# Kernel tuning notes

Hardware: AMD Instinct MI355X
Metric: run time of the kernel (lower is better)

The kernel has to match this reference:

```python
import jax, jax.numpy as jnp
import numpy as np

H = 16      # num_attention_heads
HKV = 4     # num_key_value_heads
HIDDEN = 1024
HEAD_DIM = HIDDEN // H  # 64
ROPE_BASE = 10000.0


def _rope(x):
    # Rotate-half RoPE applied over the FULL projected last dim, matching the
    # module which applies self._rope before splitting into heads.
    B, S, D = x.shape
    half = D // 2
    inv_freq = 1.0 / (ROPE_BASE ** (jnp.arange(half, dtype=jnp.float32) / half))
    ang = jnp.arange(S, dtype=jnp.float32)[:, None] * inv_freq[None, :]  # [S, half]
    cos, sin = jnp.cos(ang), jnp.sin(ang)
    x1, x2 = x[..., :half], x[..., half:]
    return jnp.concatenate([x1 * cos - x2 * sin, x2 * cos + x1 * sin], axis=-1)


def _rmsnorm(x):
    # F.rms_norm with no weight: x / sqrt(mean(x^2) + eps)
    eps = jnp.finfo(x.dtype).eps
    return x * jax.lax.rsqrt(jnp.mean(x * x, axis=-1, keepdims=True) + eps)


def setup_inputs() -> dict:
    key = jax.random.key(0)
    ks = jax.random.split(key, 10)
    B, S = 2, 2048
    kv_dim = HKV * HEAD_DIM
    sc = 0.02
    return {
        "hidden_state": jax.random.normal(ks[0], (B, S, HIDDEN), dtype=jnp.float32),
        "attention_mask": jnp.zeros((B, S, S), dtype=jnp.float32),
        "Wq": jax.random.normal(ks[1], (HIDDEN, HIDDEN), dtype=jnp.float32) * sc,
        "bq": jnp.zeros((HIDDEN,), dtype=jnp.float32),
        "Wk": jax.random.normal(ks[2], (HIDDEN, kv_dim), dtype=jnp.float32) * sc,
        "bk": jnp.zeros((kv_dim,), dtype=jnp.float32),
        "Wv": jax.random.normal(ks[3], (HIDDEN, kv_dim), dtype=jnp.float32) * sc,
        "bv": jnp.zeros((kv_dim,), dtype=jnp.float32),
        "Wo": jax.random.normal(ks[4], (HIDDEN, HIDDEN), dtype=jnp.float32) * sc,
        "bo": jnp.zeros((HIDDEN,), dtype=jnp.float32),
    }


def reference(hidden_state, attention_mask, Wq, bq, Wk, bk, Wv, bv, Wo, bo):
    B, S, _ = hidden_state.shape
    G = H // HKV  # query heads per kv head
    d = HEAD_DIM

    q = hidden_state @ Wq + bq            # [B,S,H*d]
    k = hidden_state @ Wk + bk            # [B,S,Hkv*d]
    v = hidden_state @ Wv + bv            # [B,S,Hkv*d]

    q = _rope(q)
    k = _rope(k)

    # split heads; repeat_interleave of KV over groups == grouping Q heads as [Hkv, G]
    q = q.reshape(B, S, H, d).transpose(0, 2, 1, 3).reshape(B, HKV, G, S, d)
    k = k.reshape(B, S, HKV, d).transpose(0, 2, 1, 3)   # [B,Hkv,S,d]
    v = v.reshape(B, S, HKV, d).transpose(0, 2, 1, 3)   # [B,Hkv,S,d]

    q = _rmsnorm(q)
    k = _rmsnorm(k)

    scale = d ** 0.5
    scores = jnp.einsum('bkgqd,bksd->bkgqs', q, k) / scale  # [B,Hkv,G,S,S]
    scores = scores + attention_mask[:, None, None, :, :]
    attn = jax.nn.softmax(scores, axis=-1)
    out = jnp.einsum('bkgqs,bksd->bkgqd', attn, v)          # [B,Hkv,G,S,d]

    out = out.reshape(B, H, S, d).transpose(0, 2, 1, 3).reshape(B, S, H * d)
    return out @ Wo + bo
```

## Files before the change

### kernel.cpp

```cpp
#include <hip/hip_runtime.h>
#include <cmath>

#define SEQ 2048
#define BATCH 2
#define HID 1024
#define NH 16
#define NKV 4
#define DH 64
#define KVDIM 256
#define K32C 32

typedef __attribute__((ext_vector_type(8))) short bf16x8;
typedef __attribute__((ext_vector_type(4))) float f32x4;

static __device__ __forceinline__ unsigned short f2bf(float x) {
  union { float f; unsigned u; } v; v.f = x;
  unsigned r = v.u + 0x7fffu + ((v.u >> 16) & 1u);
  return (unsigned short)(r >> 16);
}
static __device__ __forceinline__ float bf2f(unsigned short h) {
  union { unsigned u; float f; } v; v.u = ((unsigned)h) << 16;
  return v.f;
}
static __device__ __forceinline__ void gl_lds16(const unsigned short* g, unsigned short* l) {
  __builtin_amdgcn_global_load_lds(
      (const __attribute__((address_space(1))) unsigned int*)g,
      (__attribute__((address_space(3))) unsigned int*)l, 16, 0, 0);
}

template<bool HILO>
__global__ __launch_bounds__(256) void pack_a_kernel(
    const float* __restrict__ A, unsigned short* __restrict__ hi,
    unsigned short* __restrict__ lo) {
  int gid = blockIdx.x * 256 + threadIdx.x;
  int lane = gid & 63;
  int k32 = (gid >> 6) & 31;
  int m16 = gid >> 11;
  int quad = lane >> 4, l16 = lane & 15;
  const float* src = A + (size_t)(m16 * 16 + l16) * 1024 + k32 * 32 + quad * 8;
  float4 a0 = *(const float4*)src;
  float4 a1 = *(const float4*)(src + 4);
  float v[8] = {a0.x, a0.y, a0.z, a0.w, a1.x, a1.y, a1.z, a1.w};
  unsigned short h[8], l[8];
#pragma unroll
  for (int j = 0; j < 8; ++j) {
    h[j] = f2bf(v[j]);
    if (HILO) l[j] = f2bf(v[j] - bf2f(h[j]));
  }
  *(bf16x8*)(hi + (size_t)gid * 8) = *(bf16x8*)h;
  if (HILO) *(bf16x8*)(lo + (size_t)gid * 8) = *(bf16x8*)l;
}

__global__ __launch_bounds__(256) void pack_a_norm_kernel(
    const float* __restrict__ A, const float* __restrict__ lpart,
    unsigned short* __restrict__ hi, unsigned short* __restrict__ lo) {
  int gid = blockIdx.x * 256 + threadIdx.x;
  int lane = gid & 63;
  int k32 = (gid >> 6) & 31;
  int m16 = gid >> 11;
  int quad = lane >> 4, l16 = lane & 15;
  int m = m16 * 16 + l16;
  int b = m >> 11, s = m & 2047;
  int k0 = k32 * 32 + quad * 8;
  int h = k0 >> 6;
  float inv = 1.0f / lpart[(size_t)(b * NH + h) * SEQ + s];
  const float* src = A + (size_t)m * 1024 + k0;
  float4 a0 = *(const float4*)src;
  float4 a1 = *(const float4*)(src + 4);
  float v[8] = {a0.x, a0.y, a0.z, a0.w, a1.x, a1.y, a1.z, a1.w};
  unsigned short hh[8], ll[8];
#pragma unroll
  for (int j = 0; j < 8; ++j) {
    float x = v[j] * inv;
    hh[j] = f2bf(x);
    ll[j] = f2bf(x - bf2f(hh[j]));
  }
  *(bf16x8*)(hi + (size_t)gid * 8) = *(bf16x8*)hh;
  *(bf16x8*)(lo + (size_t)gid * 8) = *(bf16x8*)ll;
}

template<bool HILO>
__global__ __launch_bounds__(256) void pack_b_kernel(
    const float* __restrict__ W, unsigned short* __restrict__ hi,
    unsigned short* __restrict__ lo, int Nsrc) {
  int gid = blockIdx.x * 256 + threadIdx.x;
  int lane = gid & 63;
  int k32 = (gid >> 6) & 31;
  int n16 = gid >> 11;
  int quad = lane >> 4, l16 = lane & 15;
  int n = n16 * 16 + l16, k = k32 * 32 + quad * 8;
  unsigned short h[8], l[8];
#pragma unroll
  for (int j = 0; j < 8; ++j) {
    float v = W[(size_t)(k + j) * Nsrc + n];
    h[j] = f2bf(v);
    if (HILO) l[j] = f2bf(v - bf2f(h[j]));
  }
  *(bf16x8*)(hi + (size_t)gid * 8) = *(bf16x8*)h;
  if (HILO) *(bf16x8*)(lo + (size_t)gid * 8) = *(bf16x8*)l;
}

__global__ __launch_bounds__(256) void bias_cat_kernel(
    const float* __restrict__ bq, const float* __restrict__ bk,
    const float* __restrict__ bv, float* __restrict__ dst) {
  int n = blockIdx.x * 256 + threadIdx.x;
  if (n < 1536)
    dst[n] = (n < 1024) ? bq[n] : (n < 1280 ? bk[n - 1024] : bv[n - 1280]);
}

template<int CHAINS, bool OUTBF16>
__global__ __launch_bounds__(256) void gemm_pk_kernel(
    const unsigned short* __restrict__ Ah, const unsigned short* __restrict__ Al,
    const unsigned short* __restrict__ Bh, const unsigned short* __restrict__ Bl,
    const float* __restrict__ bias, void* __restrict__ Cout, int N) {
  constexpr int NCH = (CHAINS == 3) ? 2 : 1;
  __shared__ unsigned short Asm[NCH][4 * 512];
  __shared__ unsigned short Bsm[NCH][8 * 512];
  const int tid = threadIdx.x;
  const int wave = tid >> 6, lane = tid & 63;
  const int wr = wave >> 1, wc = wave & 1;
  const int quad = lane >> 4, l16 = lane & 15;
  const size_t abase = ((size_t)(blockIdx.y * 4 + wave) * K32C) * 64 + lane;
  const size_t bbase0 = ((size_t)(blockIdx.x * 8 + wave) * K32C) * 64 + lane;
  const size_t bbase1 = ((size_t)(blockIdx.x * 8 + wave + 4) * K32C) * 64 + lane;
  f32x4 acc[2][4] = {};
  for (int k32 = 0; k32 < K32C; ++k32) {
    __syncthreads();
    gl_lds16(Ah + (abase + (size_t)k32 * 64) * 8, &Asm[0][wave * 512]);
    gl_lds16(Bh + (bbase0 + (size_t)k32 * 64) * 8, &Bsm[0][wave * 512]);
    gl_lds16(Bh + (bbase1 + (size_t)k32 * 64) * 8, &Bsm[0][(wave + 4) * 512]);
    if (CHAINS == 3) {
      gl_lds16(Al + (abase + (size_t)k32 * 64) * 8, &Asm[1][wave * 512]);
      gl_lds16(Bl + (bbase0 + (size_t)k32 * 64) * 8, &Bsm[1][wave * 512]);
      gl_lds16(Bl + (bbase1 + (size_t)k32 * 64) * 8, &Bsm[1][(wave + 4) * 512]);
    }
    __syncthreads();
    bf16x8 af[2][NCH], bfr[4][NCH];
#pragma unroll
    for (int mt = 0; mt < 2; ++mt)
#pragma unroll
      for (int ch = 0; ch < NCH; ++ch)
        af[mt][ch] = *(const bf16x8*)&Asm[ch][((wr * 2 + mt) * 64 + lane) * 8];
#pragma unroll
    for (int nt = 0; nt < 4; ++nt)
#pragma unroll
      for (int ch = 0; ch < NCH; ++ch)
        bfr[nt][ch] = *(const bf16x8*)&Bsm[ch][((wc * 4 + nt) * 64 + lane) * 8];
#pragma unroll
    for (int mt = 0; mt < 2; ++mt)
#pragma unroll
      for (int nt = 0; nt < 4; ++nt) {
        acc[mt][nt] = __builtin_amdgcn_mfma_f32_16x16x32_bf16(af[mt][0], bfr[nt][0], acc[mt][nt], 0, 0, 0);
        if (CHAINS == 3) {
          acc[mt][nt] = __builtin_amdgcn_mfma_f32_16x16x32_bf16(af[mt][1], bfr[nt][0], acc[mt][nt], 0, 0, 0);
          acc[mt][nt] = __builtin_amdgcn_mfma_f32_16x16x32_bf16(af[mt][0], bfr[nt][1], acc[mt][nt], 0, 0, 0);
        }
      }
  }
  const int n0 = blockIdx.x * 128 + wc * 64;
  const int m0 = blockIdx.y * 64 + wr * 32;
#pragma unroll
  for (int mt = 0; mt < 2; ++mt)
#pragma unroll
    for (int nt = 0; nt < 4; ++nt)
#pragma unroll
      for (int r = 0; r < 4; ++r) {
        int gm = m0 + mt * 16 + quad * 4 + r;
        int n = n0 + nt * 16 + l16;
        float v = acc[mt][nt][r] + bias[n];
        if (OUTBF16)
          ((unsigned short*)Cout)[(size_t)gm * N + n] = f2bf(v);
        else
          ((float*)Cout)[(size_t)gm * N + n] = v;
      }
}

__global__ __launch_bounds__(1024) void rope_norm_q_kernel(
    const unsigned short* __restrict__ qkv, unsigned short* __restrict__ Qh,
    unsigned short* __restrict__ Ql) {
  const int s = blockIdx.x, b = blockIdx.y;
  const int t = threadIdx.x;
  const unsigned short* row = qkv + ((size_t)b * SEQ + s) * 1536;
  const int j = t & 511;
  float invf = exp2f((float)j * (-13.287712379549449f / 512.0f));
  float ang = (float)s * invf;
  float c = cosf(ang), sn = sinf(ang);
  float x1 = bf2f(row[j]), x2 = bf2f(row[j + 512]);
  float val = (t < 512) ? (x1 * c - x2 * sn) : (x2 * c + x1 * sn);
  float ss = val * val;
#pragma unroll
  for (int off = 1; off < 64; off <<= 1) ss += __shfl_xor(ss, off);
  float rn = rsqrtf(ss * (1.0f / 64.0f) + 1.1920929e-07f);
  float v = val * rn;
  unsigned short hi = f2bf(v);
  unsigned short lo = f2bf(v - bf2f(hi));
  int h = t >> 6, d = t & 63;
  size_t o = (size_t)(b * NH + h) * 131072 +
             ((((size_t)(s >> 4) * 2 + (d >> 5)) * 64) + ((d >> 3) & 3) * 16 + (s & 15)) * 8 + (d & 7);
  Qh[o] = hi;
  Ql[o] = lo;
}

__global__ __launch_bounds__(256) void rope_norm_kv_kernel(
    const unsigned short* __restrict__ qkv, unsigned short* __restrict__ Kpk,
    unsigned short* __restrict__ Vpk) {
  const int s = blockIdx.x, b = blockIdx.y;
  const int t = threadIdx.x;
  const unsigned short* row = qkv + ((size_t)b * SEQ + s) * 1536;
  const int j = t & 127;
  float invf = exp2f((float)j * (-13.287712379549449f / 128.0f));
  float ang = (float)s * invf;
  float c = cosf(ang), sn = sinf(ang);
  float x1 = bf2f(row[1024 + j]), x2 = bf2f(row[1024 + 128 + j]);
  float val = (t < 128) ? (x1 * c - x2 * sn) : (x2 * c + x1 * sn);
  float ss = val * val;
#pragma unroll
  for (int off = 1; off < 64; off <<= 1) ss += __shfl_xor(ss, off);
  float rn = rsqrtf(ss * (1.0f / 64.0f) + 1.1920929e-07f);
  float kv = val * rn;
  int h = t >> 6, d = t & 63;
  size_t ko = (size_t)(b * NKV + h) * 131072 +
              ((((size_t)(s >> 4) * 2 + (d >> 5)) * 64) + ((d >> 3) & 3) * 16 + (s & 15)) * 8 + (d & 7);
  Kpk[ko] = f2bf(kv);
  size_t vo = (size_t)(b * NKV + h) * 131072 +
              ((((size_t)(d >> 4) * 64 + (s >> 5)) * 64) + ((s >> 3) & 3) * 16 + (d & 15)) * 8 + (s & 7);
  Vpk[vo] = row[1280 + t];
}

__global__ __launch_bounds__(256, 3) void attn_mfma3_kernel(
    const unsigned short* __restrict__ Qh, const unsigned short* __restrict__ Ql,
    const unsigned short* __restrict__ Kpk, const unsigned short* __restrict__ Vpk,
    const float* __restrict__ mask, float* __restrict__ attn_po,
    float* __restrict__ l_part) {
  __shared__ unsigned short Ps[4][32 * 72];

  const int b = blockIdx.z;
  const int kvh = blockIdx.y >> 1, jh = blockIdx.y & 1;
  const int q0 = blockIdx.x * 32;
  const int tid = threadIdx.x, wave = tid >> 6, lane = tid & 63;
  const int quad = lane >> 4, l16 = lane & 15;
  const int h = kvh * 4 + wave;

  bf16x8 qh[2][2], ql[2][2];
  {
    const unsigned short* Qb_h = Qh + (size_t)(b * NH + h) * 131072;
    const unsigned short* Qb_l = Ql + (size_t)(b * NH + h) * 131072;
#pragma unroll
    for (int mt = 0; mt < 2; ++mt)
#pragma unroll
      for (int kf = 0; kf < 2; ++kf) {
        size_t o = ((((size_t)(q0 >> 4) + mt) * 2 + kf) * 64 + lane) * 8;
        qh[mt][kf] = *(const bf16x8*)(Qb_h + o);
        ql[mt][kf] = *(const bf16x8*)(Qb_l + o);
      }
  }

  const unsigned short* Kbase = Kpk + (size_t)(b * NKV + kvh) * 131072;
  const unsigned short* Vbase = Vpk + (size_t)(b * NKV + kvh) * 131072;
  const float* mbase = mask + ((size_t)b * SEQ + q0) * SEQ;

  bf16x8 ones;
#pragma unroll
  for (int i = 0; i < 8; ++i) ones[i] = (short)0x3F80;

  f32x4 O[2][4] = {};
  f32x4 lAcc[2] = {};

  const int jbase = jh * (SEQ / 2);
  constexpr float SC = 0.18033688011112042f;
  constexpr float L2E = 1.4426950408889634f;
  constexpr float MOFF = -11.541560327111707f;

  for (int jc = 0; jc < 32; ++jc) {
    const int j0 = jbase + jc * 32;

    bf16x8 kbf[2][2], vbf[4];
#pragma unroll
    for (int nt = 0; nt < 2; ++nt)
#pragma unroll
      for (int kf = 0; kf < 2; ++kf)
        kbf[nt][kf] = *(const bf16x8*)(Kbase +
            ((((size_t)(j0 >> 4) + nt) * 2 + kf) * 64 + lane) * 8);
#pragma unroll
    for (int d16 = 0; d16 < 4; ++d16)
      vbf[d16] = *(const bf16x8*)(Vbase +
          (((size_t)d16 * 64 + (j0 >> 5)) * 64 + lane) * 8);

#pragma unroll
    for (int mt = 0; mt < 2; ++mt)
#pragma unroll
      for (int nt = 0; nt < 2; ++nt) {
        f32x4 C = {};
        C = __builtin_amdgcn_mfma_f32_16x16x32_bf16(qh[mt][0], kbf[nt][0], C, 0, 0, 0);
        C = __builtin_amdgcn_mfma_f32_16x16x32_bf16(qh[mt][1], kbf[nt][1], C, 0, 0, 0);
        C = __builtin_amdgcn_mfma_f32_16x16x32_bf16(ql[mt][0], kbf[nt][0], C, 0, 0, 0);
        C = __builtin_amdgcn_mfma_f32_16x16x32_bf16(ql[mt][1], kbf[nt][1], C, 0, 0, 0);
#pragma unroll
        for (int r = 0; r < 4; ++r) {
          int row = mt * 16 + quad * 4 + r;
          float m = mbase[(size_t)row * SEQ + j0 + nt * 16 + l16];
          float p = exp2f(fmaf(C[r], SC, fmaf(m, L2E, MOFF)));
          union { float f; unsigned u; } pu; pu.f = p;
          Ps[wave][row * 72 + nt * 16 + l16] = (unsigned short)((pu.u + 0x8000u) >> 16);
        }
      }

    bf16x8 pa[2];
#pragma unroll
    for (int mt = 0; mt < 2; ++mt)
      pa[mt] = *(const bf16x8*)&Ps[wave][(mt * 16 + l16) * 72 + quad * 8];
#pragma unroll
    for (int mt = 0; mt < 2; ++mt) {
      lAcc[mt] = __builtin_amdgcn_mfma_f32_16x16x32_bf16(pa[mt], ones, lAcc[mt], 0, 0, 0);
#pragma unroll
      for (int nt = 0; nt < 4; ++nt)
        O[mt][nt] = __builtin_amdgcn_mfma_f32_16x16x32_bf16(pa[mt], vbf[nt], O[mt][nt], 0, 0, 0);
    }
  }

#pragma unroll
  for (int mt = 0; mt < 2; ++mt)
#pragma unroll
    for (int r = 0; r < 4; ++r) {
      int s = q0 + mt * 16 + quad * 4 + r;
#pragma unroll
      for (int nt = 0; nt < 4; ++nt)
        atomicAdd(attn_po + ((size_t)b * SEQ + s) * HID + h * DH + nt * 16 + l16,
                  O[mt][nt][r]);
      if (l16 == 0)
        atomicAdd(l_part + (size_t)(b * NH + h) * SEQ + s, lAcc[mt][r]);
    }
}

extern "C" void kernel_launch(void* const* d_in, const int* in_sizes, int n_in,
                              void* d_out, int out_size, void* d_ws, size_t ws_size,
                              hipStream_t stream) {
  const float* hs   = (const float*)d_in[0];
  const float* mask = (const float*)d_in[1];
  const float* Wq   = (const float*)d_in[2];
  const float* bq   = (const float*)d_in[3];
  const float* Wk   = (const float*)d_in[4];
  const float* bk   = (const float*)d_in[5];
  const float* Wv   = (const float*)d_in[6];
  const float* bv   = (const float*)d_in[7];
  const float* Wo   = (const float*)d_in[8];
  const float* bo   = (const float*)d_in[9];
  float* out = (float*)d_out;
  char* ws = (char*)d_ws;
  const size_t MiB = 1048576;

  unsigned short* hs_pk   = (unsigned short*)(ws);
  unsigned short* qkvproj = (unsigned short*)(ws + 8 * MiB);
  float*          attn_po = (float*)(ws);
  float*          l_part  = (float*)(ws + 16 * MiB);
  unsigned short* Wqkv_hi = (unsigned short*)(ws + 20 * MiB);
  unsigned short* Wo_hi   = (unsigned short*)(ws + 20 * MiB);
  unsigned short* Wo_lo   = (unsigned short*)(ws + 22 * MiB);
  unsigned short* Qpk_h   = (unsigned short*)(ws + 24 * MiB);
  unsigned short* Qpk_l   = (unsigned short*)(ws + 32 * MiB);
  unsigned short* ao_hi   = (unsigned short*)(ws + 24 * MiB);
  unsigned short* ao_lo   = (unsigned short*)(ws + 32 * MiB);
  unsigned short* Kpk     = (unsigned short*)(ws + 40 * MiB);
  unsigned short* Vpk     = (unsigned short*)(ws + 42 * MiB);
  float*          bias_c  = (float*)(ws + 44 * MiB);

  pack_a_kernel<false><<<2048, 256, 0, stream>>>(hs, hs_pk, nullptr);
  pack_b_kernel<false><<<512, 256, 0, stream>>>(Wq, Wqkv_hi, nullptr, 1024);
  pack_b_kernel<false><<<128, 256, 0, stream>>>(Wk, Wqkv_hi + (size_t)64 * 2048 * 8, nullptr, 256);
  pack_b_kernel<false><<<128, 256, 0, stream>>>(Wv, Wqkv_hi + (size_t)80 * 2048 * 8, nullptr, 256);
  bias_cat_kernel<<<6, 256, 0, stream>>>(bq, bk, bv, bias_c);

  gemm_pk_kernel<1, true><<<dim3(12, 64), 256, 0, stream>>>(
      hs_pk, nullptr, Wqkv_hi, nullptr, bias_c, qkvproj, 1536);

  pack_b_kernel<true><<<512, 256, 0, stream>>>(Wo, Wo_hi, Wo_lo, 1024);

  rope_norm_q_kernel<<<dim3(SEQ, BATCH), dim3(1024), 0, stream>>>(qkvproj, Qpk_h, Qpk_l);
  rope_norm_kv_kernel<<<dim3(SEQ, BATCH), dim3(256), 0, stream>>>(qkvproj, Kpk, Vpk);

  hipMemsetAsync(ws, 0, 16 * MiB + 262144, stream);
  attn_mfma3_kernel<<<dim3(SEQ / 32, NKV * 2, BATCH), 256, 0, stream>>>(
      Qpk_h, Qpk_l, Kpk, Vpk, mask, attn_po, l_part);

  pack_a_norm_kernel<<<2048, 256, 0, stream>>>(attn_po, l_part, ao_hi, ao_lo);
  gemm_pk_kernel<3, false><<<dim3(8, 64), 256, 0, stream>>>(
      ao_hi, ao_lo, Wo_hi, Wo_lo, bo, out, 1024);
}
```

Baseline: 306.1 us.

## Compute transposed scores to keep P in registers, drop LDS staging

```diff
diff --git a/kernel.cpp b/kernel.cpp
--- a/kernel.cpp
+++ b/kernel.cpp
@@ -52,7 +52,7 @@
 }
 
 __global__ __launch_bounds__(256) void pack_a_norm_kernel(
-    const float* __restrict__ A, const float* __restrict__ lpart,
+    const float* __restrict__ At, const float* __restrict__ lpart,
     unsigned short* __restrict__ hi, unsigned short* __restrict__ lo) {
   int gid = blockIdx.x * 256 + threadIdx.x;
   int lane = gid & 63;
@@ -62,16 +62,13 @@
   int m = m16 * 16 + l16;
   int b = m >> 11, s = m & 2047;
   int k0 = k32 * 32 + quad * 8;
-  int h = k0 >> 6;
+  int h = k0 >> 6, d0 = k0 & 63;
   float inv = 1.0f / lpart[(size_t)(b * NH + h) * SEQ + s];
-  const float* src = A + (size_t)m * 1024 + k0;
-  float4 a0 = *(const float4*)src;
-  float4 a1 = *(const float4*)(src + 4);
-  float v[8] = {a0.x, a0.y, a0.z, a0.w, a1.x, a1.y, a1.z, a1.w};
+  const float* src = At + ((size_t)(b * NH + h) * DH + d0) * SEQ + s;
   unsigned short hh[8], ll[8];
 #pragma unroll
   for (int j = 0; j < 8; ++j) {
-    float x = v[j] * inv;
+    float x = src[(size_t)j * SEQ] * inv;
     hh[j] = f2bf(x);
     ll[j] = f2bf(x - bf2f(hh[j]));
   }
@@ -227,13 +224,11 @@
   Vpk[vo] = row[1280 + t];
 }
 
-__global__ __launch_bounds__(256, 3) void attn_mfma3_kernel(
+__global__ __launch_bounds__(256, 3) void attn_mfma4_kernel(
     const unsigned short* __restrict__ Qh, const unsigned short* __restrict__ Ql,
     const unsigned short* __restrict__ Kpk, const unsigned short* __restrict__ Vpk,
-    const float* __restrict__ mask, float* __restrict__ attn_po,
+    const float* __restrict__ mask, float* __restrict__ attn_pot,
     float* __restrict__ l_part) {
-  __shared__ unsigned short Ps[4][32 * 72];
-
   const int b = blockIdx.z;
   const int kvh = blockIdx.y >> 1, jh = blockIdx.y & 1;
   const int q0 = blockIdx.x * 32;
@@ -241,95 +236,123 @@
   const int quad = lane >> 4, l16 = lane & 15;
   const int h = kvh * 4 + wave;
 
-  bf16x8 qh[2][2], ql[2][2];
+  bf16x8 qbf[2][2][2];
   {
     const unsigned short* Qb_h = Qh + (size_t)(b * NH + h) * 131072;
     const unsigned short* Qb_l = Ql + (size_t)(b * NH + h) * 131072;
 #pragma unroll
-    for (int mt = 0; mt < 2; ++mt)
+    for (int qt = 0; qt < 2; ++qt)
 #pragma unroll
       for (int kf = 0; kf < 2; ++kf) {
-        size_t o = ((((size_t)(q0 >> 4) + mt) * 2 + kf) * 64 + lane) * 8;
-        qh[mt][kf] = *(const bf16x8*)(Qb_h + o);
-        ql[mt][kf] = *(const bf16x8*)(Qb_l + o);
+        size_t o = ((((size_t)(q0 >> 4) + qt) * 2 + kf) * 64 + lane) * 8;
+        qbf[qt][kf][0] = *(const bf16x8*)(Qb_h + o);
+        qbf[qt][kf][1] = *(const bf16x8*)(Qb_l + o);
       }
   }
 
-  const unsigned short* Kbase = Kpk + (size_t)(b * NKV + kvh) * 131072;
-  const unsigned short* Vbase = Vpk + (size_t)(b * NKV + kvh) * 131072;
-  const float* mbase = mask + ((size_t)b * SEQ + q0) * SEQ;
-
-  bf16x8 ones;
-#pragma unroll
-  for (int i = 0; i < 8; ++i) ones[i] = (short)0x3F80;
+  const unsigned short* Kb = Kpk + (size_t)(b * NKV + kvh) * 131072;
+  const unsigned short* Vb = Vpk + (size_t)(b * NKV + kvh) * 131072;
+  const float* mrow0 = mask + ((size_t)b * SEQ + q0 + l16) * SEQ;
+  const float* mrow1 = mrow0 + (size_t)16 * SEQ;
 
   f32x4 O[2][4] = {};
-  f32x4 lAcc[2] = {};
+  float lAcc[2] = {0.0f, 0.0f};
 
   const int jbase = jh * (SEQ / 2);
   constexpr float SC = 0.18033688011112042f;
   constexpr float L2E = 1.4426950408889634f;
   constexpr float MOFF = -11.541560327111707f;
-
+  const int idxA = ((quad & 1) << 5) + l16;
+  const int idxB = idxA + 16;
+  const bool hi2 = quad >= 2;
+
+#pragma unroll 2
   for (int jc = 0; jc < 32; ++jc) {
     const int j0 = jbase + jc * 32;
 
-    bf16x8 kbf[2][2], vbf[4];
-#pragma unroll
-    for (int nt = 0; nt < 2; ++nt)
+    bf16x8 kfr[2][2], vfr[4];
+#pragma unroll
+    for (int jt = 0; jt < 2; ++jt)
 #pragma unroll
       for (int kf = 0; kf < 2; ++kf)
-        kbf[nt][kf] = *(const bf16x8*)(Kbase +
-            ((((size_t)(j0 >> 4) + nt) * 2 + kf) * 64 + lane) * 8);
+        kfr[jt][kf] = *(const bf16x8*)(Kb +
+            ((((size_t)(j0 >> 4) + jt) * 2 + kf) * 64 + lane) * 8);
 #pragma unroll
     for (int d16 = 0; d16 < 4; ++d16)
-      vbf[d16] = *(const bf16x8*)(Vbase +
+      vfr[d16] = *(const bf16x8*)(Vb +
           (((size_t)d16 * 64 + (j0 >> 5)) * 64 + lane) * 8);
-
-#pragma unroll
-    for (int mt = 0; mt < 2; ++mt)
-#pragma unroll
-      for (int nt = 0; nt < 2; ++nt) {
+    float4 mk[2][2];
+#pragma unroll
+    for (int jt = 0; jt < 2; ++jt) {
+      mk[jt][0] = *(const float4*)(mrow0 + j0 + jt * 16 + quad * 4);
+      mk[jt][1] = *(const float4*)(mrow1 + j0 + jt * 16 + quad * 4);
+    }
+
+    unsigned pd[2][2][2];
+#pragma unroll
+    for (int jt = 0; jt < 2; ++jt)
+#pragma unroll
+      for (int qt = 0; qt < 2; ++qt) {
         f32x4 C = {};
-        C = __builtin_amdgcn_mfma_f32_16x16x32_bf16(qh[mt][0], kbf[nt][0], C, 0, 0, 0);
-        C = __builtin_amdgcn_mfma_f32_16x16x32_bf16(qh[mt][1], kbf[nt][1], C, 0, 0, 0);
-        C = __builtin_amdgcn_mfma_f32_16x16x32_bf16(ql[mt][0], kbf[nt][0], C, 0, 0, 0);
-        C = __builtin_amdgcn_mfma_f32_16x16x32_bf16(ql[mt][1], kbf[nt][1], C, 0, 0, 0);
+        C = __builtin_amdgcn_mfma_f32_16x16x32_bf16(kfr[jt][0], qbf[qt][0][0], C, 0, 0, 0);
+        C = __builtin_amdgcn_mfma_f32_16x16x32_bf16(kfr[jt][1], qbf[qt][1][0], C, 0, 0, 0);
+        C = __builtin_amdgcn_mfma_f32_16x16x32_bf16(kfr[jt][0], qbf[qt][0][1], C, 0, 0, 0);
+        C = __builtin_amdgcn_mfma_f32_16x16x32_bf16(kfr[jt][1], qbf[qt][1][1], C, 0, 0, 0);
+        float4 m = mk[jt][qt];
+        float ms[4] = {m.x, m.y, m.z, m.w};
+        unsigned short us[4];
 #pragma unroll
         for (int r = 0; r < 4; ++r) {
-          int row = mt * 16 + quad * 4 + r;
-          float m = mbase[(size_t)row * SEQ + j0 + nt * 16 + l16];
-          float p = exp2f(fmaf(C[r], SC, fmaf(m, L2E, MOFF)));
-          union { float f; unsigned u; } pu; pu.f = p;
-          Ps[wave][row * 72 + nt * 16 + l16] = (unsigned short)((pu.u + 0x8000u) >> 16);
+          float p = exp2f(fmaf(C[r], SC, fmaf(ms[r], L2E, MOFF)));
+          us[r] = f2bf(p);
+          lAcc[qt] += bf2f(us[r]);
         }
+        pd[jt][qt][0] = (unsigned)us[0] | ((unsigned)us[1] << 16);
+        pd[jt][qt][1] = (unsigned)us[2] | ((unsigned)us[3] << 16);
       }
 
-    bf16x8 pa[2];
-#pragma unroll
-    for (int mt = 0; mt < 2; ++mt)
-      pa[mt] = *(const bf16x8*)&Ps[wave][(mt * 16 + l16) * 72 + quad * 8];
-#pragma unroll
-    for (int mt = 0; mt < 2; ++mt) {
-      lAcc[mt] = __builtin_amdgcn_mfma_f32_16x16x32_bf16(pa[mt], ones, lAcc[mt], 0, 0, 0);
-#pragma unroll
-      for (int nt = 0; nt < 4; ++nt)
-        O[mt][nt] = __builtin_amdgcn_mfma_f32_16x16x32_bf16(pa[mt], vbf[nt], O[mt][nt], 0, 0, 0);
+#pragma unroll
+    for (int qt = 0; qt < 2; ++qt) {
+      unsigned a0 = (unsigned)__shfl((int)pd[0][qt][0], idxA);
+      unsigned b0 = (unsigned)__shfl((int)pd[1][qt][0], idxA);
+      unsigned a1 = (unsigned)__shfl((int)pd[0][qt][1], idxA);
+      unsigned b1 = (unsigned)__shfl((int)pd[1][qt][1], idxA);
+      unsigned a2 = (unsigned)__shfl((int)pd[0][qt][0], idxB);
+      unsigned b2 = (unsigned)__shfl((int)pd[1][qt][0], idxB);
+      unsigned a3 = (unsigned)__shfl((int)pd[0][qt][1], idxB);
+      unsigned b3 = (unsigned)__shfl((int)pd[1][qt][1], idxB);
+      union { unsigned u[4]; bf16x8 v; } pf;
+      pf.u[0] = hi2 ? b0 : a0;
+      pf.u[1] = hi2 ? b1 : a1;
+      pf.u[2] = hi2 ? b2 : a2;
+      pf.u[3] = hi2 ? b3 : a3;
+#pragma unroll
+      for (int d16 = 0; d16 < 4; ++d16)
+        O[qt][d16] = __builtin_amdgcn_mfma_f32_16x16x32_bf16(vfr[d16], pf.v, O[qt][d16], 0, 0, 0);
     }
   }
 
 #pragma unroll
-  for (int mt = 0; mt < 2; ++mt)
-#pragma unroll
-    for (int r = 0; r < 4; ++r) {
-      int s = q0 + mt * 16 + quad * 4 + r;
-#pragma unroll
-      for (int nt = 0; nt < 4; ++nt)
-        atomicAdd(attn_po + ((size_t)b * SEQ + s) * HID + h * DH + nt * 16 + l16,
-                  O[mt][nt][r]);
-      if (l16 == 0)
-        atomicAdd(l_part + (size_t)(b * NH + h) * SEQ + s, lAcc[mt][r]);
-    }
+  for (int qt = 0; qt < 2; ++qt) {
+    lAcc[qt] += __shfl_xor(lAcc[qt], 16);
+    lAcc[qt] += __shfl_xor(lAcc[qt], 32);
+  }
+  if (quad == 0) {
+#pragma unroll
+    for (int qt = 0; qt < 2; ++qt)
+      atomicAdd(l_part + (size_t)(b * NH + h) * SEQ + q0 + qt * 16 + l16, lAcc[qt]);
+  }
+
+#pragma unroll
+  for (int qt = 0; qt < 2; ++qt)
+#pragma unroll
+    for (int d16 = 0; d16 < 4; ++d16)
+#pragma unroll
+      for (int r = 0; r < 4; ++r) {
+        int d = d16 * 16 + quad * 4 + r;
+        atomicAdd(attn_pot + ((size_t)(b * NH + h) * DH + d) * SEQ + q0 + qt * 16 + l16,
+                  O[qt][d16][r]);
+      }
 }
 
 extern "C" void kernel_launch(void* const* d_in, const int* in_sizes, int n_in,
@@ -351,7 +374,7 @@
 
   unsigned short* hs_pk   = (unsigned short*)(ws);
   unsigned short* qkvproj = (unsigned short*)(ws + 8 * MiB);
-  float*          attn_po = (float*)(ws);
+  float*          attn_pot= (float*)(ws);
   float*          l_part  = (float*)(ws + 16 * MiB);
   unsigned short* Wqkv_hi = (unsigned short*)(ws + 20 * MiB);
   unsigned short* Wo_hi   = (unsigned short*)(ws + 20 * MiB);
@@ -379,10 +402,10 @@
   rope_norm_kv_kernel<<<dim3(SEQ, BATCH), dim3(256), 0, stream>>>(qkvproj, Kpk, Vpk);
 
   hipMemsetAsync(ws, 0, 16 * MiB + 262144, stream);
-  attn_mfma3_kernel<<<dim3(SEQ / 32, NKV * 2, BATCH), 256, 0, stream>>>(
-      Qpk_h, Qpk_l, Kpk, Vpk, mask, attn_po, l_part);
-
-  pack_a_norm_kernel<<<2048, 256, 0, stream>>>(attn_po, l_part, ao_hi, ao_lo);
+  attn_mfma4_kernel<<<dim3(SEQ / 32, NKV * 2, BATCH), 256, 0, stream>>>(
+      Qpk_h, Qpk_l, Kpk, Vpk, mask, attn_pot, l_part);
+
+  pack_a_norm_kernel<<<2048, 256, 0, stream>>>(attn_pot, l_part, ao_hi, ao_lo);
   gemm_pk_kernel<3, false><<<dim3(8, 64), 256, 0, stream>>>(
       ao_hi, ao_lo, Wo_hi, Wo_lo, bo, out, 1024);
 }
```

Result: slower. 353.2 us (+15.4%).
